# Performance work log

Hardware: AMD Instinct MI355X
Metric: run time of the kernel (lower is better)

Reference implementation:

```python
import jax, jax.numpy as jnp
import numpy as np

NUM_HEADS = 12
SCRA_SCALING = 10.0
EPS = 1e-12  # F.normalize default eps


def setup_inputs() -> dict:
    key = jax.random.key(0)
    ks = jax.random.split(key, 5)
    B, N, C = 2, 2048, 768
    return {
        "x": jax.random.normal(ks[0], (B, N, C), dtype=jnp.float32),
        "qkv_w": jax.random.normal(ks[1], (3 * C, C), dtype=jnp.float32) * 0.02,
        "qkv_b": jax.random.normal(ks[2], (3 * C,), dtype=jnp.float32) * 0.02,
        "proj_w": jax.random.normal(ks[3], (C, C), dtype=jnp.float32) * 0.02,
        "proj_b": jax.random.normal(ks[4], (C,), dtype=jnp.float32) * 0.02,
    }


def reference(x, qkv_w, qkv_b, proj_w, proj_b):
    B, N, C = x.shape
    H = NUM_HEADS
    D = C // H
    scale = D ** -0.5

    xt = jnp.transpose(x, (1, 0, 2))  # [N, B, C]
    qkv = xt @ qkv_w.T + qkv_b        # [N, B, 3C]
    q, k, v = jnp.split(qkv, 3, axis=-1)

    def to_bh(t):  # [N, B, C] -> [B*H, N, D]
        return jnp.transpose(t.reshape(N, B * H, D), (1, 0, 2))

    q, k, v = to_bh(q), to_bh(k), to_bh(v)

    # Stage 1: standard attention
    attn = jax.nn.softmax(jnp.einsum('bnd,bmd->bnm', q, k) * scale, axis=-1)
    out = jnp.einsum('bnm,bmd->bnd', attn, v)  # [B*H, N, D]
    out = jnp.transpose(out, (1, 0, 2)).reshape(N, B, C)
    out = out @ proj_w.T + proj_b              # first proj
    out = jnp.transpose(out.reshape(N, B * H, D), (1, 0, 2))  # [B*H, N, D]

    # Stage 2: self-correlation attention with data-dependent masking
    norm = jnp.linalg.norm(out, axis=-1, keepdims=True)
    sim_tokens = out / jnp.maximum(norm, EPS)
    sim = jnp.einsum('bnd,bmd->bnm', sim_tokens, sim_tokens) * SCRA_SCALING
    sim = jnp.where(sim < 0, -jnp.inf, sim)
    sim = jax.nn.softmax(sim, axis=-1)
    out2 = jnp.einsum('bnm,bmd->bnd', sim, v)
    out2 = jnp.transpose(out2, (1, 0, 2)).reshape(N, B, C)
    out2 = out2 @ proj_w.T + proj_b            # second proj (same weights)

    return jnp.transpose(out2, (1, 0, 2))      # [B, N, C]
```

## Files before the change

kernel.cpp:

```cpp
#include <hip/hip_runtime.h>

typedef unsigned short u16;
typedef __bf16 bf16_t;
typedef bf16_t bf16x8 __attribute__((ext_vector_type(8)));
typedef float f32x4 __attribute__((ext_vector_type(4)));

static __device__ __forceinline__ u16 f2bf(float f) {
  unsigned u = __builtin_bit_cast(unsigned, f);
  u += 0x7FFFu + ((u >> 16) & 1u);
  return (u16)(u >> 16);
}
static __device__ __forceinline__ bf16x8 ldfrag(const u16* p) {
  return __builtin_bit_cast(bf16x8, *(const uint4*)p);
}
static __device__ __forceinline__ float fexp2(float x) {
#if __has_builtin(__builtin_amdgcn_exp2f)
  return __builtin_amdgcn_exp2f(x);
#else
  return __expf(x * 0.69314718056f);
#endif
}
static __device__ __forceinline__ unsigned pack_hi16(unsigned hi, unsigned lo) {
#if __has_builtin(__builtin_amdgcn_perm)
  return __builtin_amdgcn_perm(hi, lo, 0x07060302u);
#else
  return (lo >> 16) | (hi & 0xFFFF0000u);
#endif
}
static __device__ __forceinline__ int sw(int row, int chunk) {
  return (row << 6) + ((chunk ^ (row & 7)) << 3);
}

#define QWSZ 1769472
#define PWSZ 589824

__global__ __launch_bounds__(256) void convert_w(
    const float* __restrict__ qw, const float* __restrict__ pw,
    u16* __restrict__ qwb, u16* __restrict__ pwb)
{
  const int i = (blockIdx.x * 256 + threadIdx.x) * 8;
  const float* src; u16* dst; int off;
  if (i < QWSZ) { src = qw; dst = qwb; off = i; }
  else { src = pw; dst = pwb; off = i - QWSZ; }
  float4 a = *(const float4*)(src + off), b = *(const float4*)(src + off + 4);
  u16 t[8] = {f2bf(a.x), f2bf(a.y), f2bf(a.z), f2bf(a.w),
              f2bf(b.x), f2bf(b.y), f2bf(b.z), f2bf(b.w)};
  *(uint4*)(dst + off) = *(const uint4*)t;
}

template<int MODE>
__global__ __launch_bounds__(256, 2) void gemm_nt(
    const void* __restrict__ Araw, const u16* __restrict__ W,
    const float* __restrict__ bias,
    u16* __restrict__ d0, float* __restrict__ df)
{
  constexpr int BM = (MODE == 0) ? 128 : 64;
  constexpr int MI = (MODE == 0) ? 4 : 2;
  __shared__ __align__(16) u16 sA[BM * 64];
  __shared__ __align__(16) u16 sB[128 * 64];
  const float* Af = (const float*)Araw;
  const u16*   Ab = (const u16*)Araw;
  const int tid = threadIdx.x;
  const int m0 = blockIdx.y * BM, n0 = blockIdx.x * 128;
  const int w = tid >> 6, lane = tid & 63, l16 = lane & 15, quad = lane >> 4;
  const int wm = (w >> 1) * (BM / 2), wn = (w & 1) * 64;

  f32x4 acc[MI][4] = {};
  const int sr = tid >> 3, sc = (tid & 7) * 8, ch = tid & 7;

  for (int k0 = 0; k0 < 768; k0 += 64) {
    #pragma unroll
    for (int rr = 0; rr < BM; rr += 32) {
      if (MODE == 0) {
        const float* ap = Af + (size_t)(m0 + sr + rr) * 768 + k0 + sc;
        float4 a = *(const float4*)ap, b = *(const float4*)(ap + 4);
        u16 t[8] = {f2bf(a.x), f2bf(a.y), f2bf(a.z), f2bf(a.w),
                    f2bf(b.x), f2bf(b.y), f2bf(b.z), f2bf(b.w)};
        *(uint4*)(sA + sw(sr + rr, ch)) = *(const uint4*)t;
      } else {
        *(uint4*)(sA + sw(sr + rr, ch)) =
            *(const uint4*)(Ab + (size_t)(m0 + sr + rr) * 768 + k0 + sc);
      }
    }
    #pragma unroll
    for (int rr = 0; rr < 128; rr += 32)
      *(uint4*)(sB + sw(sr + rr, ch)) =
          *(const uint4*)(W + (size_t)(n0 + sr + rr) * 768 + k0 + sc);
    __syncthreads();
    #pragma unroll
    for (int ks = 0; ks < 2; ks++) {
      bf16x8 af[MI], bfv[4];
      #pragma unroll
      for (int i = 0; i < MI; i++)
        af[i] = ldfrag(sA + sw(wm + i * 16 + l16, ks * 4 + quad));
      #pragma unroll
      for (int i = 0; i < 4; i++)
        bfv[i] = ldfrag(sB + sw(wn + i * 16 + l16, ks * 4 + quad));
      #pragma unroll
      for (int mi = 0; mi < MI; mi++)
        #pragma unroll
        for (int ni = 0; ni < 4; ni++)
          acc[mi][ni] = __builtin_amdgcn_mfma_f32_16x16x32_bf16(af[mi], bfv[ni], acc[mi][ni], 0, 0, 0);
    }
    __syncthreads();
  }

  if (MODE == 0) {
    #pragma unroll
    for (int ni = 0; ni < 4; ni++) {
      const int gn = n0 + wn + ni * 16 + l16;
      const float bv = bias[gn];
      #pragma unroll
      for (int mi = 0; mi < MI; mi++) {
        #pragma unroll
        for (int r = 0; r < 4; r++) {
          const int gm = m0 + wm + mi * 16 + quad * 4 + r;
          const float v = acc[mi][ni][r] + bv;
          const int which = gn / 768, c = gn - which * 768, h = c >> 6, d = c & 63;
          const int b = gm >> 11, nt = gm & 2047;
          u16* dst = d0 + (size_t)which * 3145728;
          dst[(((size_t)(b * 12 + h)) * 2048 + nt) * 64 + d] = f2bf(v);
        }
      }
    }
  } else if (MODE == 1) {
    #pragma unroll
    for (int mi = 0; mi < MI; mi++) {
      #pragma unroll
      for (int r = 0; r < 4; r++) {
        float v[4]; float ss = 0.f;
        #pragma unroll
        for (int ni = 0; ni < 4; ni++) {
          v[ni] = acc[mi][ni][r] + bias[n0 + wn + ni * 16 + l16];
          ss += v[ni] * v[ni];
        }
        #pragma unroll
        for (int off = 1; off < 16; off <<= 1) ss += __shfl_xor(ss, off);
        const float scl = 1.f / fmaxf(sqrtf(ss), 1e-12f);
        const int gm = m0 + wm + mi * 16 + quad * 4 + r;
        const int nt = gm >> 1, b = gm & 1;
        #pragma unroll
        for (int ni = 0; ni < 4; ni++) {
          const int gn = n0 + wn + ni * 16 + l16, h = gn >> 6, d = gn & 63;
          d0[(((size_t)(b * 12 + h)) * 2048 + nt) * 64 + d] = f2bf(v[ni] * scl);
        }
      }
    }
  } else {
    #pragma unroll
    for (int ni = 0; ni < 4; ni++) {
      const int gn = n0 + wn + ni * 16 + l16;
      const float bv = bias[gn];
      #pragma unroll
      for (int mi = 0; mi < MI; mi++) {
        #pragma unroll
        for (int r = 0; r < 4; r++) {
          const int gm = m0 + wm + mi * 16 + quad * 4 + r;
          const int nt = gm >> 1, b = gm & 1;
          df[((size_t)b * 2048 + nt) * 768 + gn] = acc[mi][ni][r] + bv;
        }
      }
    }
  }
}

__global__ __launch_bounds__(256) void transpose_v(const u16* __restrict__ in,
                                                   u16* __restrict__ out)
{
  constexpr int N = 2048;
  __shared__ __align__(16) u16 t[64 * 72];
  const int bh = blockIdx.y, n0 = blockIdx.x * 64;
  const int r = threadIdx.x >> 2, c0 = (threadIdx.x & 3) * 8;
  const u16* ip = in + ((size_t)bh * N + n0 + r) * 64;
  *(uint4*)(t + r * 72 + c0)      = *(const uint4*)(ip + c0);
  *(uint4*)(t + r * 72 + c0 + 32) = *(const uint4*)(ip + c0 + 32);
  __syncthreads();
  #pragma unroll
  for (int half = 0; half < 2; half++) {
    const int cc = c0 + half * 32;
    __align__(16) u16 tmp[8];
    #pragma unroll
    for (int i = 0; i < 8; i++) tmp[i] = t[(cc + i) * 72 + r];
    *(uint4*)(out + ((size_t)bh * 64 + r) * N + n0 + cc) = *(const uint4*)tmp;
  }
}

template<int MODE>
__global__ __launch_bounds__(256, 3) void flash_attn(
    const u16* __restrict__ Qm, const u16* __restrict__ Km,
    const u16* __restrict__ VT, u16* __restrict__ Ob)
{
  constexpr int N = 2048;
  __shared__ __align__(16) u16 sU[64 * 64];
  __shared__ __align__(16) u16 sK[2][64 * 64];
  __shared__ __align__(16) u16 sVT[2][64 * 64];
  const int tid = threadIdx.x;
  const int bh = blockIdx.y, m0 = blockIdx.x * 64;
  const int b = bh / 12, h = bh % 12;
  const int w = tid >> 6, lane = tid & 63, l16 = lane & 15, quad = lane >> 4;

  constexpr float SC = (MODE == 1) ? 0.18033688011112042f
                                   : 14.426950408889634f;
  constexpr float M0 = (MODE == 1) ? 24.f : 14.6f;

  const int sr_ = tid >> 2, c0 = tid & 3;
  const u16* kbase = Km + (size_t)bh * N * 64;
  const u16* vbase = VT + (size_t)bh * 64 * N;
  {
    const u16* qp = Qm + ((size_t)bh * N + m0 + sr_) * 64;
    *(uint4*)(sU + sw(sr_, c0))     = *(const uint4*)(qp + c0 * 8);
    *(uint4*)(sU + sw(sr_, c0 + 4)) = *(const uint4*)(qp + c0 * 8 + 32);
    const u16* kp = kbase + (size_t)sr_ * 64;
    *(uint4*)(sK[0] + sw(sr_, c0))     = *(const uint4*)(kp + c0 * 8);
    *(uint4*)(sK[0] + sw(sr_, c0 + 4)) = *(const uint4*)(kp + c0 * 8 + 32);
    const u16* vp = vbase + (size_t)sr_ * N;
    *(uint4*)(sVT[0] + sw(sr_, c0))     = *(const uint4*)(vp + c0 * 8);
    *(uint4*)(sVT[0] + sw(sr_, c0 + 4)) = *(const uint4*)(vp + c0 * 8 + 32);
  }
  __syncthreads();
  bf16x8 qf0 = ldfrag(sU + sw(w * 16 + l16, quad));
  bf16x8 qf1 = ldfrag(sU + sw(w * 16 + l16, quad + 4));
  asm volatile("s_waitcnt lgkmcnt(0)" ::: "memory");

  bf16x8 ones;
  #pragma unroll
  for (int i = 0; i < 8; i++) ones[i] = (bf16_t)1.0f;

  f32x4 oacc[4] = {};
  f32x4 lacc = {};

  for (int it = 0; it < 32; it++) {
    const int buf = it & 1;
    const u16* sKb = sK[buf];
    const u16* sVb = sVT[buf];
    u16* sKn = sK[buf ^ 1];
    u16* sVn = sVT[buf ^ 1];

    uint4 pk0, pk1, pv0, pv1;
    const bool pre = (it + 1 < 32);
    if (pre) {
      const int j1 = (it + 1) * 64;
      const u16* kp = kbase + (size_t)(j1 + sr_) * 64;
      pk0 = *(const uint4*)(kp + c0 * 8);
      pk1 = *(const uint4*)(kp + c0 * 8 + 32);
      const u16* vp = vbase + (size_t)sr_ * N + j1;
      pv0 = *(const uint4*)(vp + c0 * 8);
      pv1 = *(const uint4*)(vp + c0 * 8 + 32);
    }

    f32x4 s[4];
    #pragma unroll
    for (int jt = 0; jt < 4; jt++) {
      f32x4 a = {};
      bf16x8 kf0 = ldfrag(sKb + sw(jt * 16 + l16, quad));
      bf16x8 kf1 = ldfrag(sKb + sw(jt * 16 + l16, quad + 4));
      a = __builtin_amdgcn_mfma_f32_16x16x32_bf16(kf0, qf0, a, 0, 0, 0);
      a = __builtin_amdgcn_mfma_f32_16x16x32_bf16(kf1, qf1, a, 0, 0, 0);
      s[jt] = a;
    }

    u16* sPw = sU;
    #pragma unroll
    for (int jt = 0; jt < 4; jt++) {
      unsigned pu[4];
      #pragma unroll
      for (int r = 0; r < 4; r++) {
        const float a = s[jt][r];
        float p = fexp2(fmaf(a, SC, -M0));
        if (MODE == 2 && a < 0.f) p = 0.f;
        pu[r] = __builtin_bit_cast(unsigned, p) & 0xFFFF0000u;
      }
      uint2 pk;
      pk.x = pack_hi16(pu[1], pu[0]);
      pk.y = pack_hi16(pu[3], pu[2]);
      *(uint2*)(sPw + sw(w * 16 + l16, 2 * jt + (quad >> 1)) + (quad & 1) * 4) = pk;
    }

    asm volatile("s_waitcnt lgkmcnt(0)" ::: "memory");
    bf16x8 pf0 = ldfrag(sPw + sw(w * 16 + l16, quad));
    bf16x8 pf1 = ldfrag(sPw + sw(w * 16 + l16, quad + 4));

    if (pre) {
      *(uint4*)(sKn + sw(sr_, c0))     = pk0;
      *(uint4*)(sKn + sw(sr_, c0 + 4)) = pk1;
      *(uint4*)(sVn + sw(sr_, c0))     = pv0;
      *(uint4*)(sVn + sw(sr_, c0 + 4)) = pv1;
    }

    #pragma unroll
    for (int d4 = 0; d4 < 4; d4++) {
      bf16x8 v0 = ldfrag(sVb + sw(d4 * 16 + l16, quad));
      bf16x8 v1 = ldfrag(sVb + sw(d4 * 16 + l16, quad + 4));
      oacc[d4] = __builtin_amdgcn_mfma_f32_16x16x32_bf16(v0, pf0, oacc[d4], 0, 0, 0);
      oacc[d4] = __builtin_amdgcn_mfma_f32_16x16x32_bf16(v1, pf1, oacc[d4], 0, 0, 0);
    }
    lacc = __builtin_amdgcn_mfma_f32_16x16x32_bf16(ones, pf0, lacc, 0, 0, 0);
    lacc = __builtin_amdgcn_mfma_f32_16x16x32_bf16(ones, pf1, lacc, 0, 0, 0);
    __syncthreads();
  }

  const int query = m0 + w * 16 + l16;
  const float inv = 1.f / fmaxf(lacc[0], 1e-30f);
  u16* obase = Ob + ((size_t)query * 2 + b) * 768 + h * 64;
  #pragma unroll
  for (int d4 = 0; d4 < 4; d4++) {
    u16 t[4];
    #pragma unroll
    for (int r = 0; r < 4; r++) t[r] = f2bf(oacc[d4][r] * inv);
    *(uint2*)(obase + d4 * 16 + quad * 4) = *(const uint2*)t;
  }
}

extern "C" void kernel_launch(void* const* d_in, const int* in_sizes, int n_in,
                              void* d_out, int out_size, void* d_ws, size_t ws_size,
                              hipStream_t stream) {
  const float* x      = (const float*)d_in[0];
  const float* qkv_w  = (const float*)d_in[1];
  const float* qkv_b  = (const float*)d_in[2];
  const float* proj_w = (const float*)d_in[3];
  const float* proj_b = (const float*)d_in[4];
  float* out = (float*)d_out;

  const size_t SZ = (size_t)24 * 2048 * 64;
  char* ws = (char*)d_ws;
  u16* vtb = (u16*)ws;
  size_t off = SZ * 2;
  u16* qwb = (u16*)(ws + off); off += (size_t)QWSZ * 2;
  u16* pwb = (u16*)(ws + off); off += (size_t)PWSZ * 2;
  u16* qb  = (u16*)(ws + off); off += SZ * 2 * 3;
  u16* kb  = qb + SZ;
  u16* vb  = qb + SZ * 2;
  u16* st  = kb;
  u16* o1  = (u16*)(ws + off);
  u16* o2  = o1;

  convert_w<<<1152, 256, 0, stream>>>(qkv_w, proj_w, qwb, pwb);
  gemm_nt<0><<<dim3(18, 32), 256, 0, stream>>>(x, qwb, qkv_b, qb, nullptr);
  transpose_v<<<dim3(32, 24), 256, 0, stream>>>(vb, vtb);
  flash_attn<1><<<dim3(32, 24), 256, 0, stream>>>(qb, kb, vtb, o1);
  gemm_nt<1><<<dim3(6, 64), 256, 0, stream>>>(o1, pwb, proj_b, st, nullptr);
  flash_attn<2><<<dim3(32, 24), 256, 0, stream>>>(st, st, vtb, o2);
  gemm_nt<2><<<dim3(6, 64), 256, 0, stream>>>(o2, pwb, proj_b, nullptr, out);
}
```

Before: 236.8 us.

## Double-buffer GEMM tiles, fuse V transpose into QKV epilogue, widen attention per-warp tiles

```diff
diff --git a/kernel.cpp b/kernel.cpp
--- a/kernel.cpp
+++ b/kernel.cpp
@@ -26,6 +26,14 @@
 #else
   return (lo >> 16) | (hi & 0xFFFF0000u);
 #endif
+}
+static __device__ __forceinline__ uint4 pack8_rtz(float4 a, float4 b) {
+  uint4 o;
+  o.x = pack_hi16(__builtin_bit_cast(unsigned, a.y), __builtin_bit_cast(unsigned, a.x));
+  o.y = pack_hi16(__builtin_bit_cast(unsigned, a.w), __builtin_bit_cast(unsigned, a.z));
+  o.z = pack_hi16(__builtin_bit_cast(unsigned, b.y), __builtin_bit_cast(unsigned, b.x));
+  o.w = pack_hi16(__builtin_bit_cast(unsigned, b.w), __builtin_bit_cast(unsigned, b.z));
+  return o;
 }
 static __device__ __forceinline__ int sw(int row, int chunk) {
   return (row << 6) + ((chunk ^ (row & 7)) << 3);
@@ -49,15 +57,17 @@
 }
 
 template<int MODE>
-__global__ __launch_bounds__(256, 2) void gemm_nt(
+__global__ __launch_bounds__(256, MODE == 0 ? 2 : 3) void gemm_nt(
     const void* __restrict__ Araw, const u16* __restrict__ W,
     const float* __restrict__ bias,
-    u16* __restrict__ d0, float* __restrict__ df)
+    u16* __restrict__ d0, u16* __restrict__ d1, u16* __restrict__ d2,
+    float* __restrict__ df)
 {
   constexpr int BM = (MODE == 0) ? 128 : 64;
   constexpr int MI = (MODE == 0) ? 4 : 2;
-  __shared__ __align__(16) u16 sA[BM * 64];
-  __shared__ __align__(16) u16 sB[128 * 64];
+  constexpr int AP = BM / 32;
+  __shared__ __align__(16) u16 sA[2][BM * 64];
+  __shared__ __align__(16) u16 sB[2][128 * 64];
   const float* Af = (const float*)Araw;
   const u16*   Ab = (const u16*)Araw;
   const int tid = threadIdx.x;
@@ -66,41 +76,74 @@
   const int wm = (w >> 1) * (BM / 2), wn = (w & 1) * 64;
 
   f32x4 acc[MI][4] = {};
-  const int sr = tid >> 3, sc = (tid & 7) * 8, ch = tid & 7;
-
-  for (int k0 = 0; k0 < 768; k0 += 64) {
-    #pragma unroll
-    for (int rr = 0; rr < BM; rr += 32) {
-      if (MODE == 0) {
-        const float* ap = Af + (size_t)(m0 + sr + rr) * 768 + k0 + sc;
-        float4 a = *(const float4*)ap, b = *(const float4*)(ap + 4);
-        u16 t[8] = {f2bf(a.x), f2bf(a.y), f2bf(a.z), f2bf(a.w),
-                    f2bf(b.x), f2bf(b.y), f2bf(b.z), f2bf(b.w)};
-        *(uint4*)(sA + sw(sr + rr, ch)) = *(const uint4*)t;
-      } else {
-        *(uint4*)(sA + sw(sr + rr, ch)) =
-            *(const uint4*)(Ab + (size_t)(m0 + sr + rr) * 768 + k0 + sc);
-      }
-    }
-    #pragma unroll
-    for (int rr = 0; rr < 128; rr += 32)
-      *(uint4*)(sB + sw(sr + rr, ch)) =
-          *(const uint4*)(W + (size_t)(n0 + sr + rr) * 768 + k0 + sc);
-    __syncthreads();
+  const int sr = tid >> 3, ch = tid & 7, sc = ch * 8;
+
+  #pragma unroll
+  for (int p = 0; p < AP; p++) {
+    const int row = sr + p * 32;
+    if (MODE == 0) {
+      const float* ap = Af + (size_t)(m0 + row) * 768 + sc;
+      *(uint4*)(sA[0] + sw(row, ch)) =
+          pack8_rtz(*(const float4*)ap, *(const float4*)(ap + 4));
+    } else {
+      *(uint4*)(sA[0] + sw(row, ch)) =
+          *(const uint4*)(Ab + (size_t)(m0 + row) * 768 + sc);
+    }
+  }
+  #pragma unroll
+  for (int p = 0; p < 4; p++) {
+    const int row = sr + p * 32;
+    *(uint4*)(sB[0] + sw(row, ch)) = *(const uint4*)(W + (size_t)(n0 + row) * 768 + sc);
+  }
+  __syncthreads();
+
+  for (int kt = 0; kt < 12; kt++) {
+    const int buf = kt & 1;
+    const bool pre = (kt + 1 < 12);
+    float4 ra0[AP], ra1[AP];
+    uint4 rab[AP], rb[4];
+    if (pre) {
+      const int kc = (kt + 1) * 64 + sc;
+      #pragma unroll
+      for (int p = 0; p < AP; p++) {
+        if (MODE == 0) {
+          const float* ap = Af + (size_t)(m0 + sr + p * 32) * 768 + kc;
+          ra0[p] = *(const float4*)ap;
+          ra1[p] = *(const float4*)(ap + 4);
+        } else {
+          rab[p] = *(const uint4*)(Ab + (size_t)(m0 + sr + p * 32) * 768 + kc);
+        }
+      }
+      #pragma unroll
+      for (int p = 0; p < 4; p++)
+        rb[p] = *(const uint4*)(W + (size_t)(n0 + sr + p * 32) * 768 + kc);
+    }
     #pragma unroll
     for (int ks = 0; ks < 2; ks++) {
       bf16x8 af[MI], bfv[4];
       #pragma unroll
       for (int i = 0; i < MI; i++)
-        af[i] = ldfrag(sA + sw(wm + i * 16 + l16, ks * 4 + quad));
+        af[i] = ldfrag(sA[buf] + sw(wm + i * 16 + l16, ks * 4 + quad));
       #pragma unroll
       for (int i = 0; i < 4; i++)
-        bfv[i] = ldfrag(sB + sw(wn + i * 16 + l16, ks * 4 + quad));
+        bfv[i] = ldfrag(sB[buf] + sw(wn + i * 16 + l16, ks * 4 + quad));
       #pragma unroll
       for (int mi = 0; mi < MI; mi++)
         #pragma unroll
         for (int ni = 0; ni < 4; ni++)
           acc[mi][ni] = __builtin_amdgcn_mfma_f32_16x16x32_bf16(af[mi], bfv[ni], acc[mi][ni], 0, 0, 0);
+    }
+    if (pre) {
+      #pragma unroll
+      for (int p = 0; p < AP; p++) {
+        if (MODE == 0)
+          *(uint4*)(sA[buf ^ 1] + sw(sr + p * 32, ch)) = pack8_rtz(ra0[p], ra1[p]);
+        else
+          *(uint4*)(sA[buf ^ 1] + sw(sr + p * 32, ch)) = rab[p];
+      }
+      #pragma unroll
+      for (int p = 0; p < 4; p++)
+        *(uint4*)(sB[buf ^ 1] + sw(sr + p * 32, ch)) = rb[p];
     }
     __syncthreads();
   }
@@ -110,16 +153,24 @@
     for (int ni = 0; ni < 4; ni++) {
       const int gn = n0 + wn + ni * 16 + l16;
       const float bv = bias[gn];
-      #pragma unroll
-      for (int mi = 0; mi < MI; mi++) {
-        #pragma unroll
-        for (int r = 0; r < 4; r++) {
-          const int gm = m0 + wm + mi * 16 + quad * 4 + r;
-          const float v = acc[mi][ni][r] + bv;
-          const int which = gn / 768, c = gn - which * 768, h = c >> 6, d = c & 63;
-          const int b = gm >> 11, nt = gm & 2047;
-          u16* dst = d0 + (size_t)which * 3145728;
-          dst[(((size_t)(b * 12 + h)) * 2048 + nt) * 64 + d] = f2bf(v);
+      const int which = gn / 768;
+      const int c = gn - which * 768, hh = c >> 6, d = c & 63;
+      #pragma unroll
+      for (int mi = 0; mi < 4; mi++) {
+        const int gm0 = m0 + wm + mi * 16 + quad * 4;
+        const int bb = gm0 >> 11, nt0 = gm0 & 2047;
+        if (which == 2) {
+          u16 t[4];
+          #pragma unroll
+          for (int r = 0; r < 4; r++) t[r] = f2bf(acc[mi][ni][r] + bv);
+          *(uint2*)(d2 + (((size_t)(bb * 12 + hh)) * 64 + d) * 2048 + nt0) =
+              *(const uint2*)t;
+        } else {
+          u16* dst = (which == 0) ? d0 : d1;
+          #pragma unroll
+          for (int r = 0; r < 4; r++)
+            dst[(((size_t)(bb * 12 + hh)) * 2048 + nt0 + r) * 64 + d] =
+                f2bf(acc[mi][ni][r] + bv);
         }
       }
     }
@@ -164,29 +215,8 @@
   }
 }
 
-__global__ __launch_bounds__(256) void transpose_v(const u16* __restrict__ in,
-                                                   u16* __restrict__ out)
-{
-  constexpr int N = 2048;
-  __shared__ __align__(16) u16 t[64 * 72];
-  const int bh = blockIdx.y, n0 = blockIdx.x * 64;
-  const int r = threadIdx.x >> 2, c0 = (threadIdx.x & 3) * 8;
-  const u16* ip = in + ((size_t)bh * N + n0 + r) * 64;
-  *(uint4*)(t + r * 72 + c0)      = *(const uint4*)(ip + c0);
-  *(uint4*)(t + r * 72 + c0 + 32) = *(const uint4*)(ip + c0 + 32);
-  __syncthreads();
-  #pragma unroll
-  for (int half = 0; half < 2; half++) {
-    const int cc = c0 + half * 32;
-    __align__(16) u16 tmp[8];
-    #pragma unroll
-    for (int i = 0; i < 8; i++) tmp[i] = t[(cc + i) * 72 + r];
-    *(uint4*)(out + ((size_t)bh * 64 + r) * N + n0 + cc) = *(const uint4*)tmp;
-  }
-}
-
 template<int MODE>
-__global__ __launch_bounds__(256, 3) void flash_attn(
+__global__ __launch_bounds__(128, 2) void flash_attn(
     const u16* __restrict__ Qm, const u16* __restrict__ Km,
     const u16* __restrict__ VT, u16* __restrict__ Ob)
 {
@@ -203,31 +233,35 @@
                                    : 14.426950408889634f;
   constexpr float M0 = (MODE == 1) ? 24.f : 14.6f;
 
-  const int sr_ = tid >> 2, c0 = tid & 3;
+  const int sr2 = tid >> 1, cp = (tid & 1) * 4;
   const u16* kbase = Km + (size_t)bh * N * 64;
   const u16* vbase = VT + (size_t)bh * 64 * N;
   {
-    const u16* qp = Qm + ((size_t)bh * N + m0 + sr_) * 64;
-    *(uint4*)(sU + sw(sr_, c0))     = *(const uint4*)(qp + c0 * 8);
-    *(uint4*)(sU + sw(sr_, c0 + 4)) = *(const uint4*)(qp + c0 * 8 + 32);
-    const u16* kp = kbase + (size_t)sr_ * 64;
-    *(uint4*)(sK[0] + sw(sr_, c0))     = *(const uint4*)(kp + c0 * 8);
-    *(uint4*)(sK[0] + sw(sr_, c0 + 4)) = *(const uint4*)(kp + c0 * 8 + 32);
-    const u16* vp = vbase + (size_t)sr_ * N;
-    *(uint4*)(sVT[0] + sw(sr_, c0))     = *(const uint4*)(vp + c0 * 8);
-    *(uint4*)(sVT[0] + sw(sr_, c0 + 4)) = *(const uint4*)(vp + c0 * 8 + 32);
+    const u16* qp = Qm + ((size_t)bh * N + m0 + sr2) * 64 + cp * 8;
+    const u16* kp = kbase + (size_t)sr2 * 64 + cp * 8;
+    const u16* vp = vbase + (size_t)sr2 * N + cp * 8;
+    #pragma unroll
+    for (int j = 0; j < 4; j++) {
+      *(uint4*)(sU + sw(sr2, cp + j))     = *(const uint4*)(qp + j * 8);
+      *(uint4*)(sK[0] + sw(sr2, cp + j))  = *(const uint4*)(kp + j * 8);
+      *(uint4*)(sVT[0] + sw(sr2, cp + j)) = *(const uint4*)(vp + j * 8);
+    }
   }
   __syncthreads();
-  bf16x8 qf0 = ldfrag(sU + sw(w * 16 + l16, quad));
-  bf16x8 qf1 = ldfrag(sU + sw(w * 16 + l16, quad + 4));
+  bf16x8 qf[2][2];
+  #pragma unroll
+  for (int qg = 0; qg < 2; qg++) {
+    qf[qg][0] = ldfrag(sU + sw(w * 32 + qg * 16 + l16, quad));
+    qf[qg][1] = ldfrag(sU + sw(w * 32 + qg * 16 + l16, quad + 4));
+  }
   asm volatile("s_waitcnt lgkmcnt(0)" ::: "memory");
 
   bf16x8 ones;
   #pragma unroll
   for (int i = 0; i < 8; i++) ones[i] = (bf16_t)1.0f;
 
-  f32x4 oacc[4] = {};
-  f32x4 lacc = {};
+  f32x4 oacc[2][4] = {};
+  f32x4 lacc[2] = {};
 
   for (int it = 0; it < 32; it++) {
     const int buf = it & 1;
@@ -236,78 +270,99 @@
     u16* sKn = sK[buf ^ 1];
     u16* sVn = sVT[buf ^ 1];
 
-    uint4 pk0, pk1, pv0, pv1;
+    uint4 pk[4], pv[4];
     const bool pre = (it + 1 < 32);
     if (pre) {
       const int j1 = (it + 1) * 64;
-      const u16* kp = kbase + (size_t)(j1 + sr_) * 64;
-      pk0 = *(const uint4*)(kp + c0 * 8);
-      pk1 = *(const uint4*)(kp + c0 * 8 + 32);
-      const u16* vp = vbase + (size_t)sr_ * N + j1;
-      pv0 = *(const uint4*)(vp + c0 * 8);
-      pv1 = *(const uint4*)(vp + c0 * 8 + 32);
-    }
-
-    f32x4 s[4];
+      const u16* kp = kbase + (size_t)(j1 + sr2) * 64 + cp * 8;
+      const u16* vp = vbase + (size_t)sr2 * N + j1 + cp * 8;
+      #pragma unroll
+      for (int j = 0; j < 4; j++) {
+        pk[j] = *(const uint4*)(kp + j * 8);
+        pv[j] = *(const uint4*)(vp + j * 8);
+      }
+    }
+
+    f32x4 s[2][4];
     #pragma unroll
     for (int jt = 0; jt < 4; jt++) {
-      f32x4 a = {};
       bf16x8 kf0 = ldfrag(sKb + sw(jt * 16 + l16, quad));
       bf16x8 kf1 = ldfrag(sKb + sw(jt * 16 + l16, quad + 4));
-      a = __builtin_amdgcn_mfma_f32_16x16x32_bf16(kf0, qf0, a, 0, 0, 0);
-      a = __builtin_amdgcn_mfma_f32_16x16x32_bf16(kf1, qf1, a, 0, 0, 0);
-      s[jt] = a;
-    }
-
-    u16* sPw = sU;
-    #pragma unroll
-    for (int jt = 0; jt < 4; jt++) {
-      unsigned pu[4];
-      #pragma unroll
-      for (int r = 0; r < 4; r++) {
-        const float a = s[jt][r];
-        float p = fexp2(fmaf(a, SC, -M0));
-        if (MODE == 2 && a < 0.f) p = 0.f;
-        pu[r] = __builtin_bit_cast(unsigned, p) & 0xFFFF0000u;
-      }
-      uint2 pk;
-      pk.x = pack_hi16(pu[1], pu[0]);
-      pk.y = pack_hi16(pu[3], pu[2]);
-      *(uint2*)(sPw + sw(w * 16 + l16, 2 * jt + (quad >> 1)) + (quad & 1) * 4) = pk;
+      #pragma unroll
+      for (int qg = 0; qg < 2; qg++) {
+        f32x4 a = {};
+        a = __builtin_amdgcn_mfma_f32_16x16x32_bf16(kf0, qf[qg][0], a, 0, 0, 0);
+        a = __builtin_amdgcn_mfma_f32_16x16x32_bf16(kf1, qf[qg][1], a, 0, 0, 0);
+        s[qg][jt] = a;
+      }
+    }
+
+    #pragma unroll
+    for (int qg = 0; qg < 2; qg++) {
+      const int prow = w * 32 + qg * 16 + l16;
+      #pragma unroll
+      for (int jt = 0; jt < 4; jt++) {
+        unsigned pu[4];
+        #pragma unroll
+        for (int r = 0; r < 4; r++) {
+          const float a = s[qg][jt][r];
+          float p = fexp2(fmaf(a, SC, -M0));
+          if (MODE == 2 && a < 0.f) p = 0.f;
+          pu[r] = __builtin_bit_cast(unsigned, p) & 0xFFFF0000u;
+        }
+        uint2 pkk;
+        pkk.x = pack_hi16(pu[1], pu[0]);
+        pkk.y = pack_hi16(pu[3], pu[2]);
+        *(uint2*)(sU + sw(prow, 2 * jt + (quad >> 1)) + (quad & 1) * 4) = pkk;
+      }
     }
 
     asm volatile("s_waitcnt lgkmcnt(0)" ::: "memory");
-    bf16x8 pf0 = ldfrag(sPw + sw(w * 16 + l16, quad));
-    bf16x8 pf1 = ldfrag(sPw + sw(w * 16 + l16, quad + 4));
+    bf16x8 pf[2][2];
+    #pragma unroll
+    for (int qg = 0; qg < 2; qg++) {
+      pf[qg][0] = ldfrag(sU + sw(w * 32 + qg * 16 + l16, quad));
+      pf[qg][1] = ldfrag(sU + sw(w * 32 + qg * 16 + l16, quad + 4));
+    }
 
     if (pre) {
-      *(uint4*)(sKn + sw(sr_, c0))     = pk0;
-      *(uint4*)(sKn + sw(sr_, c0 + 4)) = pk1;
-      *(uint4*)(sVn + sw(sr_, c0))     = pv0;
-      *(uint4*)(sVn + sw(sr_, c0 + 4)) = pv1;
+      #pragma unroll
+      for (int j = 0; j < 4; j++) {
+        *(uint4*)(sKn + sw(sr2, cp + j)) = pk[j];
+        *(uint4*)(sVn + sw(sr2, cp + j)) = pv[j];
+      }
     }
 
     #pragma unroll
     for (int d4 = 0; d4 < 4; d4++) {
       bf16x8 v0 = ldfrag(sVb + sw(d4 * 16 + l16, quad));
       bf16x8 v1 = ldfrag(sVb + sw(d4 * 16 + l16, quad + 4));
-      oacc[d4] = __builtin_amdgcn_mfma_f32_16x16x32_bf16(v0, pf0, oacc[d4], 0, 0, 0);
-      oacc[d4] = __builtin_amdgcn_mfma_f32_16x16x32_bf16(v1, pf1, oacc[d4], 0, 0, 0);
-    }
-    lacc = __builtin_amdgcn_mfma_f32_16x16x32_bf16(ones, pf0, lacc, 0, 0, 0);
-    lacc = __builtin_amdgcn_mfma_f32_16x16x32_bf16(ones, pf1, lacc, 0, 0, 0);
+      #pragma unroll
+      for (int qg = 0; qg < 2; qg++) {
+        oacc[qg][d4] = __builtin_amdgcn_mfma_f32_16x16x32_bf16(v0, pf[qg][0], oacc[qg][d4], 0, 0, 0);
+        oacc[qg][d4] = __builtin_amdgcn_mfma_f32_16x16x32_bf16(v1, pf[qg][1], oacc[qg][d4], 0, 0, 0);
+      }
+    }
+    #pragma unroll
+    for (int qg = 0; qg < 2; qg++) {
+      lacc[qg] = __builtin_amdgcn_mfma_f32_16x16x32_bf16(ones, pf[qg][0], lacc[qg], 0, 0, 0);
+      lacc[qg] = __builtin_amdgcn_mfma_f32_16x16x32_bf16(ones, pf[qg][1], lacc[qg], 0, 0, 0);
+    }
     __syncthreads();
   }
 
-  const int query = m0 + w * 16 + l16;
-  const float inv = 1.f / fmaxf(lacc[0], 1e-30f);
-  u16* obase = Ob + ((size_t)query * 2 + b) * 768 + h * 64;
-  #pragma unroll
-  for (int d4 = 0; d4 < 4; d4++) {
-    u16 t[4];
-    #pragma unroll
-    for (int r = 0; r < 4; r++) t[r] = f2bf(oacc[d4][r] * inv);
-    *(uint2*)(obase + d4 * 16 + quad * 4) = *(const uint2*)t;
+  #pragma unroll
+  for (int qg = 0; qg < 2; qg++) {
+    const int query = m0 + w * 32 + qg * 16 + l16;
+    const float inv = 1.f / fmaxf(lacc[qg][0], 1e-30f);
+    u16* obase = Ob + ((size_t)query * 2 + b) * 768 + h * 64;
+    #pragma unroll
+    for (int d4 = 0; d4 < 4; d4++) {
+      u16 t[4];
+      #pragma unroll
+      for (int r = 0; r < 4; r++) t[r] = f2bf(oacc[qg][d4][r] * inv);
+      *(uint2*)(obase + d4 * 16 + quad * 4) = *(const uint2*)t;
+    }
   }
 }
 
@@ -327,18 +382,16 @@
   size_t off = SZ * 2;
   u16* qwb = (u16*)(ws + off); off += (size_t)QWSZ * 2;
   u16* pwb = (u16*)(ws + off); off += (size_t)PWSZ * 2;
-  u16* qb  = (u16*)(ws + off); off += SZ * 2 * 3;
-  u16* kb  = qb + SZ;
-  u16* vb  = qb + SZ * 2;
+  u16* qb  = (u16*)(ws + off); off += SZ * 2;
+  u16* kb  = (u16*)(ws + off); off += SZ * 2;
   u16* st  = kb;
   u16* o1  = (u16*)(ws + off);
   u16* o2  = o1;
 
   convert_w<<<1152, 256, 0, stream>>>(qkv_w, proj_w, qwb, pwb);
-  gemm_nt<0><<<dim3(18, 32), 256, 0, stream>>>(x, qwb, qkv_b, qb, nullptr);
-  transpose_v<<<dim3(32, 24), 256, 0, stream>>>(vb, vtb);
-  flash_attn<1><<<dim3(32, 24), 256, 0, stream>>>(qb, kb, vtb, o1);
-  gemm_nt<1><<<dim3(6, 64), 256, 0, stream>>>(o1, pwb, proj_b, st, nullptr);
-  flash_attn<2><<<dim3(32, 24), 256, 0, stream>>>(st, st, vtb, o2);
-  gemm_nt<2><<<dim3(6, 64), 256, 0, stream>>>(o2, pwb, proj_b, nullptr, out);
-}
+  gemm_nt<0><<<dim3(18, 32), 256, 0, stream>>>(x, qwb, qkv_b, qb, kb, vtb, nullptr);
+  flash_attn<1><<<dim3(32, 24), 128, 0, stream>>>(qb, kb, vtb, o1);
+  gemm_nt<1><<<dim3(6, 64), 256, 0, stream>>>(o1, pwb, proj_b, st, nullptr, nullptr, nullptr);
+  flash_attn<2><<<dim3(32, 24), 128, 0, stream>>>(st, st, vtb, o2);
+  gemm_nt<2><<<dim3(6, 64), 256, 0, stream>>>(o2, pwb, proj_b, nullptr, nullptr, nullptr, out);
+}
```

Result: slower. 256.3 us (+8.2%).
